# Performance work log

Measured on AMD Instinct MI355X. Metric: run time of the kernel, lower is better.

## Reference

```python
import jax, jax.numpy as jnp
import numpy as np

N = 100000      # num_nodes
E = 1600000     # num_edges
F_IN = 128      # node_feature_dim
D_IN = F_IN + 1 # +1 input_cards indicator
H = 128         # hidden dim (both layers)
NUM_CARDS = 110


def _xavier(key, shape):
    fan_out, fan_in = shape
    limit = np.sqrt(6.0 / (fan_in + fan_out))
    return jax.random.uniform(key, shape, jnp.float32, -limit, limit)


def setup_inputs() -> dict:
    key = jax.random.key(0)
    ks = jax.random.split(key, 12)
    x = jax.random.normal(ks[0], (N, F_IN), jnp.float32)
    edge_index = jax.random.randint(ks[1], (2, E), 0, N, jnp.int64)
    input_cards = jax.random.randint(ks[2], (N,), 0, 2, jnp.int32)
    # SAGEConv layer 1: lin_l (neighbors), lin_r (self), each [H, D_IN] + bias
    Wl1 = _xavier(ks[3], (H, D_IN)); bl1 = jnp.zeros((H,), jnp.float32)
    Wr1 = _xavier(ks[4], (H, D_IN)); br1 = jnp.zeros((H,), jnp.float32)
    # SAGEConv layer 2
    Wl2 = _xavier(ks[5], (H, H)); bl2 = jnp.zeros((H,), jnp.float32)
    Wr2 = _xavier(ks[6], (H, H)); br2 = jnp.zeros((H,), jnp.float32)
    # output layer: normal(0, 0.01)
    Wo = 0.01 * jax.random.normal(ks[7], (NUM_CARDS, H), jnp.float32)
    bo = jnp.zeros((NUM_CARDS,), jnp.float32)
    return {"x": x, "Wl1": Wl1, "bl1": bl1, "Wr1": Wr1, "br1": br1,
            "Wl2": Wl2, "bl2": bl2, "Wr2": Wr2, "br2": br2,
            "Wo": Wo, "bo": bo,
            "edge_index": edge_index, "input_cards": input_cards}


def _sage_conv_mean(h, src, dst, deg_inv, Wl, bl, Wr, br):
    # mean-aggregate source-node features at destination nodes
    summed = jax.ops.segment_sum(h[src], dst, num_segments=N)  # [N, d]
    mean = summed * deg_inv[:, None]
    return mean @ Wl.T + bl + h @ Wr.T + br


def reference(x, Wl1, bl1, Wr1, br1, Wl2, bl2, Wr2, br2, Wo, bo,
              edge_index, input_cards):
    src, dst = edge_index[0], edge_index[1]
    deg = jax.ops.segment_sum(jnp.ones((E,), jnp.float32), dst, num_segments=N)
    deg_inv = jnp.where(deg > 0, 1.0 / jnp.maximum(deg, 1.0), 0.0)
    h = jnp.concatenate([x, input_cards.astype(jnp.float32)[:, None]], axis=1)  # [N, D_IN]
    h = jax.nn.relu(_sage_conv_mean(h, src, dst, deg_inv, Wl1, bl1, Wr1, br1))
    h = jax.nn.relu(_sage_conv_mean(h, src, dst, deg_inv, Wl2, bl2, Wr2, br2))
    logits = h @ Wo.T + bo  # [N, NUM_CARDS]
    return logits
```

## Files before the change

### kernel.cpp

```cpp
#include <hip/hip_runtime.h>
#include <hip/hip_bf16.h>

#define N_NODES 100000
#define N_EDGES 1600000
#define HDIM    128
#define KCH     4
#define NUM_CARDS 110
#define NTILES  (N_NODES / 16)
#define GEMM_BLOCKS 1024

#define NB      196
#define MAXB    10240
#define PT      4096
#define PEPT    16

typedef __attribute__((ext_vector_type(8))) short bfrag;
typedef __attribute__((ext_vector_type(4))) float ffrag;
typedef __attribute__((ext_vector_type(2))) float f32x2;

__device__ inline unsigned short f2bf(float f) {
    __hip_bfloat16 h = __float2bfloat16(f);
    unsigned short u; __builtin_memcpy(&u, &h, 2); return u;
}
__device__ inline float bf_lo(unsigned int u) {
    unsigned int v = u << 16; float f; __builtin_memcpy(&f, &v, 4); return f;
}
__device__ inline float bf_hi(unsigned int u) {
    unsigned int v = u & 0xffff0000u; float f; __builtin_memcpy(&f, &v, 4); return f;
}


__global__ __launch_bounds__(256) void k_partition(
    const int* __restrict__ src, const int* __restrict__ dst,
    int* __restrict__ bucket_cursor, unsigned int* __restrict__ part) {
    __shared__ int hist[NB];
    __shared__ int hcur[NB];
    const int t = threadIdx.x;
    const int base = blockIdx.x * PT;
    for (int i = t; i < NB; i += 256) hist[i] = 0;
    __syncthreads();
#pragma unroll
    for (int i = 0; i < PEPT; i++) {
        int e = base + i * 256 + t;
        if (e < N_EDGES) atomicAdd(&hist[dst[e] >> 9], 1);
    }
    __syncthreads();
    for (int b = t; b < NB; b += 256) {
        int h = hist[b];
        hcur[b] = h ? atomicAdd(&bucket_cursor[b], h) : 0;
    }
    __syncthreads();
#pragma unroll
    for (int i = 0; i < PEPT; i++) {
        int e = base + i * 256 + t;
        if (e < N_EDGES) {
            int d = dst[e];
            int b = d >> 9;
            int r = atomicAdd(&hcur[b], 1);
            if (r < MAXB)
                part[(size_t)b * MAXB + r] =
                    ((unsigned int)(d & 511) << 17) | (unsigned int)src[e];
        }
    }
}

__global__ __launch_bounds__(256) void k_bucket(
    const unsigned int* __restrict__ part, const int* __restrict__ bucket_cursor,
    int* __restrict__ row_off, int* __restrict__ deg, float* __restrict__ deg_inv,
    int* __restrict__ csr_src) {
    __shared__ int degl[512];
    __shared__ int offl[512];
    __shared__ int curl[512];
    __shared__ int stmp[256];
    const int t = threadIdx.x;
    const int b = blockIdx.x;
    const int n0 = b << 9;
    const int nb = min(512, N_NODES - n0);
    const int cnt = min(bucket_cursor[b], MAXB);
    const int row0 = b * MAXB;
    const unsigned int* pb = &part[(size_t)b * MAXB];

    degl[t] = 0; degl[t + 256] = 0;
    __syncthreads();
    for (int i = t; i < cnt; i += 256)
        atomicAdd(&degl[pb[i] >> 17], 1);
    __syncthreads();
    const int a0 = degl[2 * t], a1 = degl[2 * t + 1];
    stmp[t] = a0 + a1;
    __syncthreads();
    for (int off = 1; off < 256; off <<= 1) {
        int x = (t >= off) ? stmp[t - off] : 0;
        __syncthreads();
        stmp[t] += x;
        __syncthreads();
    }
    const int excl = stmp[t] - (a0 + a1);
    offl[2 * t] = excl;          curl[2 * t] = excl;
    offl[2 * t + 1] = excl + a0; curl[2 * t + 1] = excl + a0;
    __syncthreads();
    for (int i = t; i < nb; i += 256) {
        int n = n0 + i;
        int d = degl[i];
        row_off[n] = row0 + offl[i];
        deg[n] = d;
        deg_inv[n] = (d > 0) ? 1.0f / (float)d : 0.0f;
    }
    for (int i = t; i < cnt; i += 256) {
        unsigned int pk = pb[i];
        int r = atomicAdd(&curl[pk >> 17], 1);
        csr_src[row0 + r] = (int)(pk & 0x1FFFFu);
    }
}


__global__ void k_prep_w(const float* __restrict__ Wl1, const float* __restrict__ Wr1,
                         const float* __restrict__ bl1, const float* __restrict__ br1,
                         const float* __restrict__ Wl2, const float* __restrict__ Wr2,
                         const float* __restrict__ bl2, const float* __restrict__ br2,
                         const float* __restrict__ Wo,  const float* __restrict__ bo,
                         unsigned short* __restrict__ W1, unsigned short* __restrict__ W2,
                         unsigned short* __restrict__ Wob,
                         float* __restrict__ bias1, float* __restrict__ bias2,
                         float* __restrict__ biaso, float* __restrict__ wcard1) {
    const int j = blockIdx.x;
    const int k = threadIdx.x;
    const float* s1 = (j < 128) ? &Wl1[(size_t)j * 129] : &Wr1[(size_t)(j - 128) * 129];
    W1[(size_t)j * HDIM + k] = f2bf(s1[k]);
    const float* s2 = (j < 128) ? &Wl2[(size_t)j * HDIM] : &Wr2[(size_t)(j - 128) * HDIM];
    W2[(size_t)j * HDIM + k] = f2bf(s2[k]);
    if (j < 112)
        Wob[(size_t)j * HDIM + k] = (j < NUM_CARDS) ? f2bf(Wo[(size_t)j * HDIM + k])
                                                    : (unsigned short)0;
    if (k == 0) {
        wcard1[j] = s1[HDIM];
        bias1[j] = (j < 128) ? 0.f : (bl1[j - 128] + br1[j - 128]);
        bias2[j] = (j < 128) ? 0.f : (bl2[j - 128] + br2[j - 128]);
        if (j < 112) biaso[j] = (j < NUM_CARDS) ? bo[j] : 0.f;
    }
}


__global__ __launch_bounds__(256) void k_gemm_dual(
    const unsigned short* __restrict__ Ab, const float* __restrict__ Af,
    const int* __restrict__ cards,
    const unsigned short* __restrict__ W,
    const float* __restrict__ bias, const float* __restrict__ wcard,
    unsigned char* __restrict__ Gq, unsigned short* __restrict__ Rb,
    int layer1) {
    const int wave = threadIdx.x >> 6;
    const int lane = threadIdx.x & 63;
    const int m16 = lane & 15;
    const int quad = lane >> 4;
    const int u0 = wave * 4;
    const bool isG = (wave < 2);

    bfrag wf[4][KCH];
    float bs[4][4], wc[4][4];
#pragma unroll
    for (int u = 0; u < 4; u++) {
        const int j = (u0 + u) * 16 + m16;
#pragma unroll
        for (int c = 0; c < KCH; c++)
            wf[u][c] = *(const bfrag*)&W[(size_t)j * HDIM + c * 32 + quad * 8];
#pragma unroll
        for (int r = 0; r < 4; r++) {
            const int jj = (u0 + u) * 16 + quad * 4 + r;
            bs[u][r] = bias[jj];
            wc[u][r] = layer1 ? wcard[jj] : 0.f;
        }
    }

    for (int tile = blockIdx.x; tile < NTILES; tile += GEMM_BLOCKS) {
        const int node = tile * 16 + m16;
        bfrag hf[KCH];
        float cv = 0.f;
        if (layer1) {
#pragma unroll
            for (int c = 0; c < KCH; c++) {
                const float4 p0 = *(const float4*)&Af[(size_t)node * HDIM + c * 32 + quad * 8];
                const float4 p1 = *(const float4*)&Af[(size_t)node * HDIM + c * 32 + quad * 8 + 4];
                bfrag h;
                h[0] = (short)f2bf(p0.x); h[1] = (short)f2bf(p0.y);
                h[2] = (short)f2bf(p0.z); h[3] = (short)f2bf(p0.w);
                h[4] = (short)f2bf(p1.x); h[5] = (short)f2bf(p1.y);
                h[6] = (short)f2bf(p1.z); h[7] = (short)f2bf(p1.w);
                hf[c] = h;
            }
            cv = (float)cards[node];
        } else {
#pragma unroll
            for (int c = 0; c < KCH; c++)
                hf[c] = *(const bfrag*)&Ab[(size_t)node * HDIM + c * 32 + quad * 8];
        }
#pragma unroll
        for (int u = 0; u < 4; u++) {
            ffrag acc = {0.f, 0.f, 0.f, 0.f};
#pragma unroll
            for (int c = 0; c < KCH; c++)
                acc = __builtin_amdgcn_mfma_f32_16x16x32_bf16(wf[u][c], hf[c], acc, 0, 0, 0);
            float v[4];
#pragma unroll
            for (int r = 0; r < 4; r++)
                v[r] = acc[r] + bs[u][r] + cv * wc[u][r];
            if (isG) {
                int pk = __builtin_amdgcn_cvt_pk_fp8_f32(v[0], v[1], 0, false);
                pk = __builtin_amdgcn_cvt_pk_fp8_f32(v[2], v[3], pk, true);
                *(unsigned int*)&Gq[(size_t)node * HDIM + (u0 + u) * 16 + quad * 4] =
                    (unsigned int)pk;
            } else {
                unsigned short o[4];
#pragma unroll
                for (int r = 0; r < 4; r++) o[r] = f2bf(v[r]);
                uint2 p = {(unsigned int)o[0] | ((unsigned int)o[1] << 16),
                           (unsigned int)o[2] | ((unsigned int)o[3] << 16)};
                *(uint2*)&Rb[(size_t)node * HDIM + (u0 + u - 8) * 16 + quad * 4] = p;
            }
        }
    }
}


__global__ __launch_bounds__(256) void k_agg(
    const unsigned char* __restrict__ Gq, const unsigned short* __restrict__ Rb,
    const int* __restrict__ row_off, const int* __restrict__ deg,
    const float* __restrict__ deg_inv, const int* __restrict__ csr_src,
    unsigned short* __restrict__ outH) {
    const int wave = threadIdx.x >> 6;
    const int lane = threadIdx.x & 63;
    const int g = lane >> 3;
    const int l = lane & 7;
    const int n = (blockIdx.x * 4 + wave) * 8 + g;
    const int start = row_off[n];
    const int d = deg[n];
    const float di = deg_inv[n];
    const int fo = l * 16;

    int dmax = d;
    dmax = max(dmax, __shfl_xor(dmax, 8, 64));
    dmax = max(dmax, __shfl_xor(dmax, 16, 64));
    dmax = max(dmax, __shfl_xor(dmax, 32, 64));

    const uint4 rv0 = *(const uint4*)&Rb[(size_t)n * HDIM + fo];
    const uint4 rv1 = *(const uint4*)&Rb[(size_t)n * HDIM + fo + 8];

    f32x2 acc2[8];
#pragma unroll
    for (int i = 0; i < 8; i++) acc2[i] = (f32x2){0.f, 0.f};

    int idxA = (l < d) ? csr_src[start + l] * HDIM : 0;
    int idxB = (8 + l < d) ? csr_src[start + 8 + l] * HDIM : 0;

    uint4 cur = {0u, 0u, 0u, 0u};
    {
        const int off0 = __shfl(idxA, g << 3, 64);
        if (0 < d) cur = *(const uint4*)&Gq[(size_t)(unsigned)off0 + fo];
    }
#define ACC16(Cv)                                                        \
    acc2[0] += __builtin_amdgcn_cvt_pk_f32_fp8((int)(Cv).x, false);      \
    acc2[1] += __builtin_amdgcn_cvt_pk_f32_fp8((int)(Cv).x, true);       \
    acc2[2] += __builtin_amdgcn_cvt_pk_f32_fp8((int)(Cv).y, false);      \
    acc2[3] += __builtin_amdgcn_cvt_pk_f32_fp8((int)(Cv).y, true);       \
    acc2[4] += __builtin_amdgcn_cvt_pk_f32_fp8((int)(Cv).z, false);      \
    acc2[5] += __builtin_amdgcn_cvt_pk_f32_fp8((int)(Cv).z, true);       \
    acc2[6] += __builtin_amdgcn_cvt_pk_f32_fp8((int)(Cv).w, false);      \
    acc2[7] += __builtin_amdgcn_cvt_pk_f32_fp8((int)(Cv).w, true);

    for (int i = 1; i < dmax; i++) {
        const int sl = i & 7;
        if (sl == 0) {
            idxA = idxB;
            const int j = i + 8 + l;
            idxB = (j < d) ? csr_src[start + j] * HDIM : 0;
        }
        const int offn = __shfl(idxA, (g << 3) | sl, 64);
        uint4 nxt = {0u, 0u, 0u, 0u};
        if (i < d) nxt = *(const uint4*)&Gq[(size_t)(unsigned)offn + fo];
        ACC16(cur);
        cur = nxt;
    }
    ACC16(cur);
#undef ACC16

    const float r[16] = {bf_lo(rv0.x), bf_hi(rv0.x), bf_lo(rv0.y), bf_hi(rv0.y),
                         bf_lo(rv0.z), bf_hi(rv0.z), bf_lo(rv0.w), bf_hi(rv0.w),
                         bf_lo(rv1.x), bf_hi(rv1.x), bf_lo(rv1.y), bf_hi(rv1.y),
                         bf_lo(rv1.z), bf_hi(rv1.z), bf_lo(rv1.w), bf_hi(rv1.w)};
    unsigned short o[16];
#pragma unroll
    for (int i = 0; i < 8; i++) {
        o[2 * i]     = f2bf(fmaxf(acc2[i].x * di + r[2 * i], 0.f));
        o[2 * i + 1] = f2bf(fmaxf(acc2[i].y * di + r[2 * i + 1], 0.f));
    }
    uint4 p0, p1;
    p0.x = (unsigned int)o[0] | ((unsigned int)o[1] << 16);
    p0.y = (unsigned int)o[2] | ((unsigned int)o[3] << 16);
    p0.z = (unsigned int)o[4] | ((unsigned int)o[5] << 16);
    p0.w = (unsigned int)o[6] | ((unsigned int)o[7] << 16);
    p1.x = (unsigned int)o[8] | ((unsigned int)o[9] << 16);
    p1.y = (unsigned int)o[10] | ((unsigned int)o[11] << 16);
    p1.z = (unsigned int)o[12] | ((unsigned int)o[13] << 16);
    p1.w = (unsigned int)o[14] | ((unsigned int)o[15] << 16);
    *(uint4*)&outH[(size_t)n * HDIM + fo] = p0;
    *(uint4*)&outH[(size_t)n * HDIM + fo + 8] = p1;
}


__global__ __launch_bounds__(256) void k_gemm_logits(
    const unsigned short* __restrict__ A, const unsigned short* __restrict__ W,
    const float* __restrict__ bias, float* __restrict__ out) {
    const int wave = threadIdx.x >> 6;
    const int lane = threadIdx.x & 63;
    const int m16 = lane & 15;
    const int quad = lane >> 4;
    const int u0 = wave * 2;

    bfrag wf[2][KCH];
    float bsj[2];
#pragma unroll
    for (int u = 0; u < 2; u++) {
        const int unit = u0 + u;
        const int j = (unit < 7 ? unit : 0) * 16 + m16;
#pragma unroll
        for (int c = 0; c < KCH; c++)
            wf[u][c] = *(const bfrag*)&W[(size_t)j * HDIM + c * 32 + quad * 8];
        bsj[u] = bias[j];
    }

    for (int tile = blockIdx.x; tile < NTILES; tile += GEMM_BLOCKS) {
        const int nodef = tile * 16 + m16;
        bfrag hf[KCH];
#pragma unroll
        for (int c = 0; c < KCH; c++)
            hf[c] = *(const bfrag*)&A[(size_t)nodef * HDIM + c * 32 + quad * 8];
#pragma unroll
        for (int u = 0; u < 2; u++) {
            const int unit = u0 + u;
            if (unit >= 7) break;
            ffrag acc = {0.f, 0.f, 0.f, 0.f};
#pragma unroll
            for (int c = 0; c < KCH; c++)
                acc = __builtin_amdgcn_mfma_f32_16x16x32_bf16(hf[c], wf[u][c], acc, 0, 0, 0);
            const int j = unit * 16 + m16;
            if (j < NUM_CARDS) {
#pragma unroll
                for (int r = 0; r < 4; r++) {
                    const int node = tile * 16 + quad * 4 + r;
                    out[(size_t)node * NUM_CARDS + j] = acc[r] + bsj[u];
                }
            }
        }
    }
}


static inline size_t align_up(size_t x, size_t a) { return (x + a - 1) & ~(a - 1); }

extern "C" void kernel_launch(void* const* d_in, const int* in_sizes, int n_in,
                              void* d_out, int out_size, void* d_ws, size_t ws_size,
                              hipStream_t stream) {
    const float* x   = (const float*)d_in[0];
    const float* Wl1 = (const float*)d_in[1];
    const float* bl1 = (const float*)d_in[2];
    const float* Wr1 = (const float*)d_in[3];
    const float* br1 = (const float*)d_in[4];
    const float* Wl2 = (const float*)d_in[5];
    const float* bl2 = (const float*)d_in[6];
    const float* Wr2 = (const float*)d_in[7];
    const float* br2 = (const float*)d_in[8];
    const float* Wo  = (const float*)d_in[9];
    const float* bo  = (const float*)d_in[10];
    const int* edge  = (const int*)d_in[11];
    const int* cards = (const int*)d_in[12];
    float* logits = (float*)d_out;

    const int* e_src = edge;
    const int* e_dst = edge + N_EDGES;

    char* w = (char*)d_ws;
    size_t off = 0;
    int* bucket_cursor = (int*)(w + off); off = align_up(off + 256 * 4, 512);
    unsigned int* part = (unsigned int*)(w + off); off = align_up(off + (size_t)NB * MAXB * 4, 512);
    int* row_off = (int*)(w + off); off = align_up(off + N_NODES * 4, 512);
    int* deg_i   = (int*)(w + off); off = align_up(off + N_NODES * 4, 512);
    float* dinv  = (float*)(w + off); off = align_up(off + N_NODES * 4, 512);
    int* csr_src = (int*)(w + off); off = align_up(off + (size_t)NB * MAXB * 4, 512);
    unsigned char*  Gq   = (unsigned char*)(w + off);  off = align_up(off + (size_t)N_NODES * HDIM, 512);
    unsigned short* Rb   = (unsigned short*)(w + off); off = align_up(off + (size_t)N_NODES * HDIM * 2, 512);
    unsigned short* bufH = (unsigned short*)(w + off); off = align_up(off + (size_t)N_NODES * HDIM * 2, 512);
    unsigned short* W1   = (unsigned short*)(w + off); off = align_up(off + 256 * HDIM * 2, 512);
    unsigned short* W2   = (unsigned short*)(w + off); off = align_up(off + 256 * HDIM * 2, 512);
    unsigned short* Wob  = (unsigned short*)(w + off); off = align_up(off + 112 * HDIM * 2, 512);
    float* bias1  = (float*)(w + off); off = align_up(off + 256 * 4, 512);
    float* bias2  = (float*)(w + off); off = align_up(off + 256 * 4, 512);
    float* biaso  = (float*)(w + off); off = align_up(off + 112 * 4, 512);
    float* wcard1 = (float*)(w + off); off = align_up(off + 256 * 4, 512);
    (void)ws_size; (void)n_in; (void)in_sizes; (void)out_size;

    hipMemsetAsync(bucket_cursor, 0, 256 * 4, stream);
    k_prep_w<<<256, 128, 0, stream>>>(Wl1, Wr1, bl1, br1, Wl2, Wr2, bl2, br2, Wo, bo,
                                      W1, W2, Wob, bias1, bias2, biaso, wcard1);

    const int PBLK = (N_EDGES + PT - 1) / PT;
    k_partition<<<PBLK, 256, 0, stream>>>(e_src, e_dst, bucket_cursor, part);
    k_bucket<<<NB, 256, 0, stream>>>(part, bucket_cursor,
                                     row_off, deg_i, dinv, csr_src);

    k_gemm_dual<<<GEMM_BLOCKS, 256, 0, stream>>>(nullptr, x, cards, W1, bias1, wcard1, Gq, Rb, 1);
    k_agg<<<N_NODES / 32, 256, 0, stream>>>(Gq, Rb, row_off, deg_i, dinv, csr_src, bufH);
    k_gemm_dual<<<GEMM_BLOCKS, 256, 0, stream>>>(bufH, nullptr, nullptr, W2, bias2, wcard1, Gq, Rb, 0);
    k_agg<<<N_NODES / 32, 256, 0, stream>>>(Gq, Rb, row_off, deg_i, dinv, csr_src, bufH);
    k_gemm_logits<<<GEMM_BLOCKS, 256, 0, stream>>>(bufH, Wob, biaso, logits);
}
```

Baseline: 330.7 us.

## Double-buffer GEMM input tiles in LDS via async global_load_lds with swizzle

Both the dual GEMM and the logits GEMM now stage each 16-node input tile into shared memory using global_load_lds, prefetching the next tile into a second buffer while the current one is consumed. An XOR swizzle is meant to avoid LDS bank conflicts on the fragment reads. Bias and card weights move from per-thread registers into LDS to free registers. The aim is to hide global load latency behind the MFMA work and to load tiles with contiguous, coalesced accesses. The cost is extra LDS traffic, a block-wide barrier on every iteration, and no explicit wait on the async loads (vmcnt) before the barrier, which may not be guaranteed safe.

```diff
diff --git a/kernel.cpp b/kernel.cpp
--- a/kernel.cpp
+++ b/kernel.cpp
@@ -27,6 +27,12 @@
 }
 __device__ inline float bf_hi(unsigned int u) {
     unsigned int v = u & 0xffff0000u; float f; __builtin_memcpy(&f, &v, 4); return f;
+}
+
+__device__ inline void gload_lds16(const void* g, void* l) {
+    __builtin_amdgcn_global_load_lds(
+        (const __attribute__((address_space(1))) unsigned int*)g,
+        (__attribute__((address_space(3))) unsigned int*)l, 16, 0, 0);
 }
 
 
@@ -147,38 +153,73 @@
     const float* __restrict__ bias, const float* __restrict__ wcard,
     unsigned char* __restrict__ Gq, unsigned short* __restrict__ Rb,
     int layer1) {
-    const int wave = threadIdx.x >> 6;
-    const int lane = threadIdx.x & 63;
-    const int m16 = lane & 15;
+    __shared__ __align__(16) unsigned char smem[16384 + 2048];
+    float* bias_l = (float*)(smem + 16384);
+    float* wc_l   = (float*)(smem + 16384 + 1024);
+
+    const int tix  = threadIdx.x;
+    const int wave = tix >> 6;
+    const int lane = tix & 63;
+    const int m16  = lane & 15;
     const int quad = lane >> 4;
-    const int u0 = wave * 4;
+    const int u0   = wave * 4;
     const bool isG = (wave < 2);
+    const int xk   = m16 & 7;
 
     bfrag wf[4][KCH];
-    float bs[4][4], wc[4][4];
 #pragma unroll
     for (int u = 0; u < 4; u++) {
         const int j = (u0 + u) * 16 + m16;
 #pragma unroll
         for (int c = 0; c < KCH; c++)
             wf[u][c] = *(const bfrag*)&W[(size_t)j * HDIM + c * 32 + quad * 8];
-#pragma unroll
-        for (int r = 0; r < 4; r++) {
-            const int jj = (u0 + u) * 16 + quad * 4 + r;
-            bs[u][r] = bias[jj];
-            wc[u][r] = layer1 ? wcard[jj] : 0.f;
-        }
-    }
-
-    for (int tile = blockIdx.x; tile < NTILES; tile += GEMM_BLOCKS) {
-        const int node = tile * 16 + m16;
+    }
+
+    bias_l[tix] = bias[tix];
+    wc_l[tix]   = layer1 ? wcard[tix] : 0.f;
+
+    const int sw1 = (tix ^ ((tix >> 5) & 7)) << 4;
+    const int sw2 = (tix ^ ((tix >> 4) & 7)) << 4;
+    const int ldsoff = wave << 10;
+
+    int tile = blockIdx.x;
+    if (layer1) {
+        const unsigned char* g = (const unsigned char*)Af + (size_t)tile * 8192;
+        gload_lds16(g + sw1,        smem + ldsoff);
+        gload_lds16(g + sw1 + 4096, smem + 4096 + ldsoff);
+    } else {
+        const unsigned char* g = (const unsigned char*)Ab + (size_t)tile * 4096;
+        gload_lds16(g + sw2, smem + ldsoff);
+    }
+    float cvn = layer1 ? (float)cards[tile * 16 + m16] : 0.f;
+    __syncthreads();
+
+    for (int buf = 0; tile < NTILES; tile += GEMM_BLOCKS, buf ^= 1) {
+        const int tn = tile + GEMM_BLOCKS;
+        const bool more = (tn < NTILES);
+        const float cv = cvn;
+
+        if (more) {
+            if (layer1) {
+                const unsigned char* g = (const unsigned char*)Af + (size_t)tn * 8192;
+                unsigned char* d = smem + (buf ^ 1) * 8192 + ldsoff;
+                gload_lds16(g + sw1,        d);
+                gload_lds16(g + sw1 + 4096, d + 4096);
+                cvn = (float)cards[tn * 16 + m16];
+            } else {
+                const unsigned char* g = (const unsigned char*)Ab + (size_t)tn * 4096;
+                gload_lds16(g + sw2, smem + (buf ^ 1) * 4096 + ldsoff);
+            }
+        }
+
+        const unsigned char* B = smem + buf * (layer1 ? 8192 : 4096);
         bfrag hf[KCH];
-        float cv = 0.f;
         if (layer1) {
 #pragma unroll
             for (int c = 0; c < KCH; c++) {
-                const float4 p0 = *(const float4*)&Af[(size_t)node * HDIM + c * 32 + quad * 8];
-                const float4 p1 = *(const float4*)&Af[(size_t)node * HDIM + c * 32 + quad * 8 + 4];
+                const int s0 = m16 * 32 + c * 8 + quad * 2;
+                const float4 p0 = *(const float4*)(B + (((s0    ) ^ xk) << 4));
+                const float4 p1 = *(const float4*)(B + (((s0 + 1) ^ xk) << 4));
                 bfrag h;
                 h[0] = (short)f2bf(p0.x); h[1] = (short)f2bf(p0.y);
                 h[2] = (short)f2bf(p0.z); h[3] = (short)f2bf(p0.w);
@@ -186,22 +227,29 @@
                 h[6] = (short)f2bf(p1.z); h[7] = (short)f2bf(p1.w);
                 hf[c] = h;
             }
-            cv = (float)cards[node];
         } else {
 #pragma unroll
-            for (int c = 0; c < KCH; c++)
-                hf[c] = *(const bfrag*)&Ab[(size_t)node * HDIM + c * 32 + quad * 8];
-        }
+            for (int c = 0; c < KCH; c++) {
+                const int s = m16 * 16 + c * 4 + quad;
+                hf[c] = *(const bfrag*)(B + ((s ^ xk) << 4));
+            }
+        }
+
+        const int node = tile * 16 + m16;
 #pragma unroll
         for (int u = 0; u < 4; u++) {
             ffrag acc = {0.f, 0.f, 0.f, 0.f};
 #pragma unroll
             for (int c = 0; c < KCH; c++)
                 acc = __builtin_amdgcn_mfma_f32_16x16x32_bf16(wf[u][c], hf[c], acc, 0, 0, 0);
+            const int jj0 = (u0 + u) * 16 + quad * 4;
+            const float4 b0 = *(const float4*)&bias_l[jj0];
+            const float4 w0 = *(const float4*)&wc_l[jj0];
             float v[4];
-#pragma unroll
-            for (int r = 0; r < 4; r++)
-                v[r] = acc[r] + bs[u][r] + cv * wc[u][r];
+            v[0] = acc[0] + b0.x + cv * w0.x;
+            v[1] = acc[1] + b0.y + cv * w0.y;
+            v[2] = acc[2] + b0.z + cv * w0.z;
+            v[3] = acc[3] + b0.w + cv * w0.w;
             if (isG) {
                 int pk = __builtin_amdgcn_cvt_pk_fp8_f32(v[0], v[1], 0, false);
                 pk = __builtin_amdgcn_cvt_pk_fp8_f32(v[2], v[3], pk, true);
@@ -216,6 +264,8 @@
                 *(uint2*)&Rb[(size_t)node * HDIM + (u0 + u - 8) * 16 + quad * 4] = p;
             }
         }
+
+        if (more) __syncthreads();
     }
 }
 
@@ -308,11 +358,14 @@
 __global__ __launch_bounds__(256) void k_gemm_logits(
     const unsigned short* __restrict__ A, const unsigned short* __restrict__ W,
     const float* __restrict__ bias, float* __restrict__ out) {
-    const int wave = threadIdx.x >> 6;
-    const int lane = threadIdx.x & 63;
-    const int m16 = lane & 15;
+    __shared__ __align__(16) unsigned char smem[8192];
+    const int tix  = threadIdx.x;
+    const int wave = tix >> 6;
+    const int lane = tix & 63;
+    const int m16  = lane & 15;
     const int quad = lane >> 4;
-    const int u0 = wave * 2;
+    const int u0   = wave * 2;
+    const int xk   = m16 & 7;
 
     bfrag wf[2][KCH];
     float bsj[2];
@@ -326,12 +379,32 @@
         bsj[u] = bias[j];
     }
 
-    for (int tile = blockIdx.x; tile < NTILES; tile += GEMM_BLOCKS) {
-        const int nodef = tile * 16 + m16;
+    const int sw2 = (tix ^ ((tix >> 4) & 7)) << 4;
+    const int ldsoff = wave << 10;
+
+    int tile = blockIdx.x;
+    {
+        const unsigned char* g = (const unsigned char*)A + (size_t)tile * 4096;
+        gload_lds16(g + sw2, smem + ldsoff);
+    }
+    __syncthreads();
+
+    for (int buf = 0; tile < NTILES; tile += GEMM_BLOCKS, buf ^= 1) {
+        const int tn = tile + GEMM_BLOCKS;
+        const bool more = (tn < NTILES);
+        if (more) {
+            const unsigned char* g = (const unsigned char*)A + (size_t)tn * 4096;
+            gload_lds16(g + sw2, smem + (buf ^ 1) * 4096 + ldsoff);
+        }
+
+        const unsigned char* B = smem + buf * 4096;
         bfrag hf[KCH];
 #pragma unroll
-        for (int c = 0; c < KCH; c++)
-            hf[c] = *(const bfrag*)&A[(size_t)nodef * HDIM + c * 32 + quad * 8];
+        for (int c = 0; c < KCH; c++) {
+            const int s = m16 * 16 + c * 4 + quad;
+            hf[c] = *(const bfrag*)(B + ((s ^ xk) << 4));
+        }
+
 #pragma unroll
         for (int u = 0; u < 2; u++) {
             const int unit = u0 + u;
@@ -349,6 +422,8 @@
                 }
             }
         }
+
+        if (more) __syncthreads();
     }
 }
 
```

Result: faster. 317.4 us (-4.0%).

## Fuse independent prep/partition and bucket/GEMM1 kernels; use one tile per block

Applied to the files above, without the earlier changes.

Merges weight prep with edge partitioning, and the CSR bucketing with the first dense GEMM, into single launches that dispatch on block index. This removes launch gaps and lets independent work overlap. The GEMM kernels change from persistent grid-stride loops that keep weights in registers to one tile per block, which reloads weights for every tile but gives more parallelism. The logits kernel now assigns half a tile per wave with four units each. Risks are extra weight-load traffic per tile and block imbalance in the fused grids.

```diff
diff --git a/kernel.cpp b/kernel.cpp
--- a/kernel.cpp
+++ b/kernel.cpp
@@ -7,12 +7,13 @@
 #define KCH     4
 #define NUM_CARDS 110
 #define NTILES  (N_NODES / 16)
-#define GEMM_BLOCKS 1024
 
 #define NB      196
 #define MAXB    10240
 #define PT      4096
 #define PEPT    16
+#define PBLK    ((N_EDGES + PT - 1) / PT)
+#define PREPB   128
 
 typedef __attribute__((ext_vector_type(8))) short bfrag;
 typedef __attribute__((ext_vector_type(4))) float ffrag;
@@ -30,13 +31,14 @@
 }
 
 
-__global__ __launch_bounds__(256) void k_partition(
-    const int* __restrict__ src, const int* __restrict__ dst,
-    int* __restrict__ bucket_cursor, unsigned int* __restrict__ part) {
-    __shared__ int hist[NB];
-    __shared__ int hcur[NB];
+__device__ void partition_body(
+    int bid, const int* __restrict__ src, const int* __restrict__ dst,
+    int* __restrict__ bucket_cursor, unsigned int* __restrict__ part,
+    int* smem) {
+    int* hist = smem;
+    int* hcur = hist + NB;
     const int t = threadIdx.x;
-    const int base = blockIdx.x * PT;
+    const int base = bid * PT;
     for (int i = t; i < NB; i += 256) hist[i] = 0;
     __syncthreads();
 #pragma unroll
@@ -64,16 +66,17 @@
     }
 }
 
-__global__ __launch_bounds__(256) void k_bucket(
-    const unsigned int* __restrict__ part, const int* __restrict__ bucket_cursor,
+__device__ void bucket_body(
+    int bid, const unsigned int* __restrict__ part,
+    const int* __restrict__ bucket_cursor,
     int* __restrict__ row_off, int* __restrict__ deg, float* __restrict__ deg_inv,
-    int* __restrict__ csr_src) {
-    __shared__ int degl[512];
-    __shared__ int offl[512];
-    __shared__ int curl[512];
-    __shared__ int stmp[256];
+    int* __restrict__ csr_src, int* smem) {
+    int* degl = smem;
+    int* offl = degl + 512;
+    int* curl = offl + 512;
+    int* stmp = curl + 512;
     const int t = threadIdx.x;
-    const int b = blockIdx.x;
+    const int b = bid;
     const int n0 = b << 9;
     const int nb = min(512, N_NODES - n0);
     const int cnt = min(bucket_cursor[b], MAXB);
@@ -113,17 +116,19 @@
 }
 
 
-__global__ void k_prep_w(const float* __restrict__ Wl1, const float* __restrict__ Wr1,
-                         const float* __restrict__ bl1, const float* __restrict__ br1,
-                         const float* __restrict__ Wl2, const float* __restrict__ Wr2,
-                         const float* __restrict__ bl2, const float* __restrict__ br2,
-                         const float* __restrict__ Wo,  const float* __restrict__ bo,
-                         unsigned short* __restrict__ W1, unsigned short* __restrict__ W2,
-                         unsigned short* __restrict__ Wob,
-                         float* __restrict__ bias1, float* __restrict__ bias2,
-                         float* __restrict__ biaso, float* __restrict__ wcard1) {
-    const int j = blockIdx.x;
-    const int k = threadIdx.x;
+__device__ void prep_body(
+    int bid,
+    const float* __restrict__ Wl1, const float* __restrict__ Wr1,
+    const float* __restrict__ bl1, const float* __restrict__ br1,
+    const float* __restrict__ Wl2, const float* __restrict__ Wr2,
+    const float* __restrict__ bl2, const float* __restrict__ br2,
+    const float* __restrict__ Wo,  const float* __restrict__ bo,
+    unsigned short* __restrict__ W1, unsigned short* __restrict__ W2,
+    unsigned short* __restrict__ Wob,
+    float* __restrict__ bias1, float* __restrict__ bias2,
+    float* __restrict__ biaso, float* __restrict__ wcard1) {
+    const int j = bid * 2 + (threadIdx.x >> 7);
+    const int k = threadIdx.x & 127;
     const float* s1 = (j < 128) ? &Wl1[(size_t)j * 129] : &Wr1[(size_t)(j - 128) * 129];
     W1[(size_t)j * HDIM + k] = f2bf(s1[k]);
     const float* s2 = (j < 128) ? &Wl2[(size_t)j * HDIM] : &Wr2[(size_t)(j - 128) * HDIM];
@@ -140,83 +145,126 @@
 }
 
 
-__global__ __launch_bounds__(256) void k_gemm_dual(
+template <int L1>
+__device__ void gemm_dual_body(
+    int tile,
     const unsigned short* __restrict__ Ab, const float* __restrict__ Af,
     const int* __restrict__ cards,
     const unsigned short* __restrict__ W,
     const float* __restrict__ bias, const float* __restrict__ wcard,
-    unsigned char* __restrict__ Gq, unsigned short* __restrict__ Rb,
-    int layer1) {
+    unsigned char* __restrict__ Gq, unsigned short* __restrict__ Rb) {
     const int wave = threadIdx.x >> 6;
     const int lane = threadIdx.x & 63;
-    const int m16 = lane & 15;
+    const int m16  = lane & 15;
     const int quad = lane >> 4;
-    const int u0 = wave * 4;
+    const int u0   = wave * 4;
     const bool isG = (wave < 2);
+    const int node = tile * 16 + m16;
+
+    bfrag hf[KCH];
+    float cv = 0.f;
+    if (L1) {
+#pragma unroll
+        for (int c = 0; c < KCH; c++) {
+            const float4 p0 = *(const float4*)&Af[(size_t)node * HDIM + c * 32 + quad * 8];
+            const float4 p1 = *(const float4*)&Af[(size_t)node * HDIM + c * 32 + quad * 8 + 4];
+            bfrag h;
+            h[0] = (short)f2bf(p0.x); h[1] = (short)f2bf(p0.y);
+            h[2] = (short)f2bf(p0.z); h[3] = (short)f2bf(p0.w);
+            h[4] = (short)f2bf(p1.x); h[5] = (short)f2bf(p1.y);
+            h[6] = (short)f2bf(p1.z); h[7] = (short)f2bf(p1.w);
+            hf[c] = h;
+        }
+        cv = (float)cards[node];
+    } else {
+#pragma unroll
+        for (int c = 0; c < KCH; c++)
+            hf[c] = *(const bfrag*)&Ab[(size_t)node * HDIM + c * 32 + quad * 8];
+    }
 
     bfrag wf[4][KCH];
-    float bs[4][4], wc[4][4];
+    float4 b4[4], w4[4];
 #pragma unroll
     for (int u = 0; u < 4; u++) {
         const int j = (u0 + u) * 16 + m16;
 #pragma unroll
         for (int c = 0; c < KCH; c++)
             wf[u][c] = *(const bfrag*)&W[(size_t)j * HDIM + c * 32 + quad * 8];
-#pragma unroll
-        for (int r = 0; r < 4; r++) {
-            const int jj = (u0 + u) * 16 + quad * 4 + r;
-            bs[u][r] = bias[jj];
-            wc[u][r] = layer1 ? wcard[jj] : 0.f;
+        const int jj0 = (u0 + u) * 16 + quad * 4;
+        b4[u] = *(const float4*)&bias[jj0];
+        w4[u] = L1 ? *(const float4*)&wcard[jj0] : (float4){0.f, 0.f, 0.f, 0.f};
+    }
+
+#pragma unroll
+    for (int u = 0; u < 4; u++) {
+        ffrag acc = {0.f, 0.f, 0.f, 0.f};
+#pragma unroll
+        for (int c = 0; c < KCH; c++)
+            acc = __builtin_amdgcn_mfma_f32_16x16x32_bf16(wf[u][c], hf[c], acc, 0, 0, 0);
+        float v[4];
+        v[0] = acc[0] + b4[u].x + cv * w4[u].x;
+        v[1] = acc[1] + b4[u].y + cv * w4[u].y;
+        v[2] = acc[2] + b4[u].z + cv * w4[u].z;
+        v[3] = acc[3] + b4[u].w + cv * w4[u].w;
+        if (isG) {
+            int pk = __builtin_amdgcn_cvt_pk_fp8_f32(v[0], v[1], 0, false);
+            pk = __builtin_amdgcn_cvt_pk_fp8_f32(v[2], v[3], pk, true);
+            *(unsigned int*)&Gq[(size_t)node * HDIM + (u0 + u) * 16 + quad * 4] =
+                (unsigned int)pk;
+        } else {
+            unsigned short o[4];
+#pragma unroll
+            for (int r = 0; r < 4; r++) o[r] = f2bf(v[r]);
+            uint2 p = {(unsigned int)o[0] | ((unsigned int)o[1] << 16),
+                       (unsigned int)o[2] | ((unsigned int)o[3] << 16)};
+            *(uint2*)&Rb[(size_t)node * HDIM + (u0 + u - 8) * 16 + quad * 4] = p;
         }
     }
-
-    for (int tile = blockIdx.x; tile < NTILES; tile += GEMM_BLOCKS) {
-        const int node = tile * 16 + m16;
-        bfrag hf[KCH];
-        float cv = 0.f;
-        if (layer1) {
-#pragma unroll
-            for (int c = 0; c < KCH; c++) {
-                const float4 p0 = *(const float4*)&Af[(size_t)node * HDIM + c * 32 + quad * 8];
-                const float4 p1 = *(const float4*)&Af[(size_t)node * HDIM + c * 32 + quad * 8 + 4];
-                bfrag h;
-                h[0] = (short)f2bf(p0.x); h[1] = (short)f2bf(p0.y);
-                h[2] = (short)f2bf(p0.z); h[3] = (short)f2bf(p0.w);
-                h[4] = (short)f2bf(p1.x); h[5] = (short)f2bf(p1.y);
-                h[6] = (short)f2bf(p1.z); h[7] = (short)f2bf(p1.w);
-                hf[c] = h;
-            }
-            cv = (float)cards[node];
-        } else {
-#pragma unroll
-            for (int c = 0; c < KCH; c++)
-                hf[c] = *(const bfrag*)&Ab[(size_t)node * HDIM + c * 32 + quad * 8];
-        }
-#pragma unroll
-        for (int u = 0; u < 4; u++) {
-            ffrag acc = {0.f, 0.f, 0.f, 0.f};
-#pragma unroll
-            for (int c = 0; c < KCH; c++)
-                acc = __builtin_amdgcn_mfma_f32_16x16x32_bf16(wf[u][c], hf[c], acc, 0, 0, 0);
-            float v[4];
-#pragma unroll
-            for (int r = 0; r < 4; r++)
-                v[r] = acc[r] + bs[u][r] + cv * wc[u][r];
-            if (isG) {
-                int pk = __builtin_amdgcn_cvt_pk_fp8_f32(v[0], v[1], 0, false);
-                pk = __builtin_amdgcn_cvt_pk_fp8_f32(v[2], v[3], pk, true);
-                *(unsigned int*)&Gq[(size_t)node * HDIM + (u0 + u) * 16 + quad * 4] =
-                    (unsigned int)pk;
-            } else {
-                unsigned short o[4];
-#pragma unroll
-                for (int r = 0; r < 4; r++) o[r] = f2bf(v[r]);
-                uint2 p = {(unsigned int)o[0] | ((unsigned int)o[1] << 16),
-                           (unsigned int)o[2] | ((unsigned int)o[3] << 16)};
-                *(uint2*)&Rb[(size_t)node * HDIM + (u0 + u - 8) * 16 + quad * 4] = p;
-            }
-        }
-    }
+}
+
+
+__global__ __launch_bounds__(256) void k_prep_part(
+    const float* __restrict__ Wl1, const float* __restrict__ Wr1,
+    const float* __restrict__ bl1, const float* __restrict__ br1,
+    const float* __restrict__ Wl2, const float* __restrict__ Wr2,
+    const float* __restrict__ bl2, const float* __restrict__ br2,
+    const float* __restrict__ Wo,  const float* __restrict__ bo,
+    unsigned short* __restrict__ W1, unsigned short* __restrict__ W2,
+    unsigned short* __restrict__ Wob,
+    float* __restrict__ bias1, float* __restrict__ bias2,
+    float* __restrict__ biaso, float* __restrict__ wcard1,
+    const int* __restrict__ e_src, const int* __restrict__ e_dst,
+    int* __restrict__ bucket_cursor, unsigned int* __restrict__ part) {
+    __shared__ int smem[2 * NB];
+    if (blockIdx.x < PREPB)
+        prep_body(blockIdx.x, Wl1, Wr1, bl1, br1, Wl2, Wr2, bl2, br2, Wo, bo,
+                  W1, W2, Wob, bias1, bias2, biaso, wcard1);
+    else
+        partition_body(blockIdx.x - PREPB, e_src, e_dst, bucket_cursor, part, smem);
+}
+
+__global__ __launch_bounds__(256) void k_bucket_gemm1(
+    const unsigned int* __restrict__ part, const int* __restrict__ bucket_cursor,
+    int* __restrict__ row_off, int* __restrict__ deg, float* __restrict__ deg_inv,
+    int* __restrict__ csr_src,
+    const float* __restrict__ Af, const int* __restrict__ cards,
+    const unsigned short* __restrict__ W,
+    const float* __restrict__ bias, const float* __restrict__ wcard,
+    unsigned char* __restrict__ Gq, unsigned short* __restrict__ Rb) {
+    __shared__ int smem[512 * 3 + 256];
+    if (blockIdx.x < NB)
+        bucket_body(blockIdx.x, part, bucket_cursor, row_off, deg, deg_inv,
+                    csr_src, smem);
+    else
+        gemm_dual_body<1>(blockIdx.x - NB, nullptr, Af, cards, W, bias, wcard,
+                          Gq, Rb);
+}
+
+__global__ __launch_bounds__(256) void k_gemm2(
+    const unsigned short* __restrict__ Ab, const unsigned short* __restrict__ W,
+    const float* __restrict__ bias,
+    unsigned char* __restrict__ Gq, unsigned short* __restrict__ Rb) {
+    gemm_dual_body<0>(blockIdx.x, Ab, nullptr, nullptr, W, bias, nullptr, Gq, Rb);
 }
 
 
@@ -310,43 +358,38 @@
     const float* __restrict__ bias, float* __restrict__ out) {
     const int wave = threadIdx.x >> 6;
     const int lane = threadIdx.x & 63;
-    const int m16 = lane & 15;
+    const int m16  = lane & 15;
     const int quad = lane >> 4;
-    const int u0 = wave * 2;
-
-    bfrag wf[2][KCH];
-    float bsj[2];
-#pragma unroll
-    for (int u = 0; u < 2; u++) {
+    const int gwid = blockIdx.x * 4 + wave;
+    const int tile = gwid >> 1;
+    const int half = gwid & 1;
+    const int u0   = half * 4;
+    const int nodef = tile * 16 + m16;
+
+    bfrag hf[KCH];
+#pragma unroll
+    for (int c = 0; c < KCH; c++)
+        hf[c] = *(const bfrag*)&A[(size_t)nodef * HDIM + c * 32 + quad * 8];
+
+#pragma unroll
+    for (int u = 0; u < 4; u++) {
         const int unit = u0 + u;
-        const int j = (unit < 7 ? unit : 0) * 16 + m16;
+        if (unit >= 7) break;
+        const int j = unit * 16 + m16;
+        bfrag wfu[KCH];
 #pragma unroll
         for (int c = 0; c < KCH; c++)
-            wf[u][c] = *(const bfrag*)&W[(size_t)j * HDIM + c * 32 + quad * 8];
-        bsj[u] = bias[j];
-    }
-
-    for (int tile = blockIdx.x; tile < NTILES; tile += GEMM_BLOCKS) {
-        const int nodef = tile * 16 + m16;
-        bfrag hf[KCH];
+            wfu[c] = *(const bfrag*)&W[(size_t)j * HDIM + c * 32 + quad * 8];
+        const float bsj = bias[j];
+        ffrag acc = {0.f, 0.f, 0.f, 0.f};
 #pragma unroll
         for (int c = 0; c < KCH; c++)
-            hf[c] = *(const bfrag*)&A[(size_t)nodef * HDIM + c * 32 + quad * 8];
-#pragma unroll
-        for (int u = 0; u < 2; u++) {
-            const int unit = u0 + u;
-            if (unit >= 7) break;
-            ffrag acc = {0.f, 0.f, 0.f, 0.f};
-#pragma unroll
-            for (int c = 0; c < KCH; c++)
-                acc = __builtin_amdgcn_mfma_f32_16x16x32_bf16(hf[c], wf[u][c], acc, 0, 0, 0);
-            const int j = unit * 16 + m16;
-            if (j < NUM_CARDS) {
-#pragma unroll
-                for (int r = 0; r < 4; r++) {
-                    const int node = tile * 16 + quad * 4 + r;
-                    out[(size_t)node * NUM_CARDS + j] = acc[r] + bsj[u];
-                }
+            acc = __builtin_amdgcn_mfma_f32_16x16x32_bf16(hf[c], wfu[c], acc, 0, 0, 0);
+        if (j < NUM_CARDS) {
+#pragma unroll
+            for (int r = 0; r < 4; r++) {
+                const int node = tile * 16 + quad * 4 + r;
+                out[(size_t)node * NUM_CARDS + j] = acc[r] + bsj;
             }
         }
     }
@@ -397,17 +440,17 @@
     (void)ws_size; (void)n_in; (void)in_sizes; (void)out_size;
 
     hipMemsetAsync(bucket_cursor, 0, 256 * 4, stream);
-    k_prep_w<<<256, 128, 0, stream>>>(Wl1, Wr1, bl1, br1, Wl2, Wr2, bl2, br2, Wo, bo,
-                                      W1, W2, Wob, bias1, bias2, biaso, wcard1);
-
-    const int PBLK = (N_EDGES + PT - 1) / PT;
-    k_partition<<<PBLK, 256, 0, stream>>>(e_src, e_dst, bucket_cursor, part);
-    k_bucket<<<NB, 256, 0, stream>>>(part, bucket_cursor,
-                                     row_off, deg_i, dinv, csr_src);
-
-    k_gemm_dual<<<GEMM_BLOCKS, 256, 0, stream>>>(nullptr, x, cards, W1, bias1, wcard1, Gq, Rb, 1);
+
+    k_prep_part<<<PREPB + PBLK, 256, 0, stream>>>(
+        Wl1, Wr1, bl1, br1, Wl2, Wr2, bl2, br2, Wo, bo,
+        W1, W2, Wob, bias1, bias2, biaso, wcard1,
+        e_src, e_dst, bucket_cursor, part);
+    k_bucket_gemm1<<<NB + NTILES, 256, 0, stream>>>(
+        part, bucket_cursor, row_off, deg_i, dinv, csr_src,
+        x, cards, W1, bias1, wcard1, Gq, Rb);
+
     k_agg<<<N_NODES / 32, 256, 0, stream>>>(Gq, Rb, row_off, deg_i, dinv, csr_src, bufH);
-    k_gemm_dual<<<GEMM_BLOCKS, 256, 0, stream>>>(bufH, nullptr, nullptr, W2, bias2, wcard1, Gq, Rb, 0);
+    k_gemm2<<<NTILES, 256, 0, stream>>>(bufH, W2, bias2, Gq, Rb);
     k_agg<<<N_NODES / 32, 256, 0, stream>>>(Gq, Rb, row_off, deg_i, dinv, csr_src, bufH);
-    k_gemm_logits<<<GEMM_BLOCKS, 256, 0, stream>>>(bufH, Wob, biaso, logits);
-}
+    k_gemm_logits<<<NTILES / 2, 256, 0, stream>>>(bufH, Wob, biaso, logits);
+}
```

New measurement: 394.9 us. +19.4%, slower.
